# Kernel optimization log

Hardware: AMD Instinct MI355X
Metric: run time of the kernel (lower is better)

The kernel has to match this reference:

```python
import jax, jax.numpy as jnp
import numpy as np
import math

NUM_BINS, NUM_FREQS, NUM_KERNELS, MLP_HIDDEN = 128, 64, 3, 64
NUM_KEYS = 8192
ANCHORS = jnp.array([1000.0, 10000.0, 100000.0], dtype=jnp.float32)
LOG_ANCHORS = jnp.log10(ANCHORS)


def setup_inputs() -> dict:
    key = jax.random.key(0)
    ks = jax.random.split(key, 12)
    K = jax.random.normal(ks[0], (NUM_KEYS, 2 * NUM_FREQS), dtype=jnp.float32)
    key_positions = jax.random.randint(ks[1], (NUM_KEYS,), 0, 131072, dtype=jnp.int32)
    reference_angles = jax.random.normal(ks[2], (NUM_FREQS,), dtype=jnp.float32)
    # KernelEncodingLayer params
    centers = jnp.array([2 * math.pi * m / NUM_KERNELS - math.pi for m in range(NUM_KERNELS)], dtype=jnp.float32)
    mu = jax.random.normal(ks[3], (NUM_BINS, NUM_FREQS, NUM_KERNELS), dtype=jnp.float32) * 0.1 + centers
    kappa = jnp.ones((NUM_BINS, NUM_FREQS, NUM_KERNELS), dtype=jnp.float32)
    weight = jax.random.normal(ks[4], (NUM_BINS, NUM_FREQS, NUM_KERNELS), dtype=jnp.float32) * 0.1
    bias = jnp.zeros((NUM_BINS,), dtype=jnp.float32)
    # MLP params (kaiming-uniform-ish init)
    lim1 = 1.0 / math.sqrt(NUM_BINS)
    W1 = jax.random.uniform(ks[5], (MLP_HIDDEN, NUM_BINS), jnp.float32, -lim1, lim1)
    b1 = jax.random.uniform(ks[6], (MLP_HIDDEN,), jnp.float32, -lim1, lim1)
    lim2 = 1.0 / math.sqrt(MLP_HIDDEN)
    W2 = jax.random.uniform(ks[7], (1, MLP_HIDDEN), jnp.float32, -lim2, lim2)
    b2 = jax.random.uniform(ks[8], (1,), jnp.float32, -lim2, lim2)
    # PositionScalingLayer: softplus^-1(1.0)
    anchor_raw = jnp.full((3,), math.log(math.exp(1.0) - 1), dtype=jnp.float32)
    return {"K": K, "key_positions": key_positions, "reference_angles": reference_angles,
            "mu": mu, "kappa": kappa, "weight": weight, "bias": bias,
            "W1": W1, "b1": b1, "W2": W2, "b2": b2, "anchor_raw": anchor_raw}


def _position_weights(positions, anchor_raw):
    aw = jax.nn.softplus(anchor_raw)  # (3,)
    log_pos = jnp.log10(jnp.maximum(positions.astype(jnp.float32), 1.0))  # (N,)
    w = jnp.full_like(log_pos, aw[0])
    for i in range(LOG_ANCHORS.shape[0] - 1):
        ll, lr = LOG_ANCHORS[i], LOG_ANCHORS[i + 1]
        t = (log_pos - ll) / (lr - ll)
        interp = aw[i] * (1 - t) + aw[i + 1] * t
        w = jnp.where((log_pos >= ll) & (log_pos < lr), interp, w)
    w = jnp.where(log_pos >= LOG_ANCHORS[-1], aw[-1], w)
    return w


def reference(K, key_positions, reference_angles, mu, kappa, weight, bias, W1, b1, W2, b2, anchor_raw):
    N = K.shape[0]
    Kc = K.reshape(N, NUM_FREQS, 2)            # (N, F, 2)
    magnitude = jnp.linalg.norm(Kc, axis=2)     # (N, F)
    angle = jnp.arctan2(Kc[..., 1], Kc[..., 0])  # (N, F)
    mu_eff = mu + reference_angles[None, :, None]  # (B, F, M)
    # von Mises kernel: (N, B, F, M)
    kern = jnp.exp(kappa[None] * (jnp.cos(angle[:, None, :, None] - mu_eff[None]) - 1.0))
    wk = jnp.einsum('nbfm,bfm->nbf', kern, weight)       # sum over kernels
    logits = jnp.einsum('nbf,nf->nb', wk, magnitude) + bias  # (N, B)
    h = jax.nn.relu(logits @ W1.T + b1)
    mlp_out = (h @ W2.T + b2)[:, 0]            # (N,)
    pos_w = _position_weights(key_positions, anchor_raw)
    return jax.nn.sigmoid(mlp_out * pos_w)
```

## Files before the change

### kernel.cpp

```cpp
#include <hip/hip_runtime.h>
#include <math.h>

#define NBINS 128
#define NFREQ 64
#define NH    4
#define NSEG  (2*NH+1)
#define KDIM  (NSEG*NFREQ)
#define KSTEPS (KDIM/32)
#define ROWF  (KDIM+8)
#define ROWL  (NBINS+8)
#define ROWP  68

typedef _Float16 f16x8 __attribute__((ext_vector_type(8)));
typedef _Float16 f16x2 __attribute__((ext_vector_type(2)));
typedef float    f32x4 __attribute__((ext_vector_type(4)));

#define MFMA16(A,B,C) __builtin_amdgcn_mfma_f32_16x16x32_f16((A),(B),(C),0,0,0)

__global__ __launch_bounds__(256) void prep_kernel(
    const float* __restrict__ mu, const float* __restrict__ kappa,
    const float* __restrict__ weight, const float* __restrict__ ref,
    const float* __restrict__ W1,
    _Float16* __restrict__ Cfrag, _Float16* __restrict__ W1h)
{
    int u = blockIdx.x * 256 + threadIdx.x;
    W1h[u] = (_Float16)W1[u];

    int f = u >> 7;
    int bin = u & 127;
    float ra = ref[f];
    float A[NH + 1], B[NH + 1];
    #pragma unroll
    for (int k = 0; k <= NH; ++k) { A[k] = 0.f; B[k] = 0.f; }

    for (int m = 0; m < 3; ++m) {
        int idx = (bin * NFREQ + f) * 3 + m;
        float kap = kappa[idx];
        float wgt = weight[idx];
        float mue = mu[idx] + ra;
        float I[NH + 1];
        float x2 = kap * 0.5f, x2sq = x2 * x2;
        float fact = 1.f, xk = 1.f;
        #pragma unroll
        for (int k = 0; k <= NH; ++k) {
            if (k > 0) { fact *= (float)k; xk *= x2; }
            float term = xk / fact;
            float s = term;
            for (int j = 1; j <= 12; ++j) {
                term *= x2sq / ((float)j * (float)(j + k));
                s += term;
            }
            I[k] = s;
        }
        float e = expf(-kap) * wgt;
        float c1, s1; sincosf(mue, &s1, &c1);
        float ck = 1.f, sk = 0.f;
        A[0] += e * I[0];
        #pragma unroll
        for (int k = 1; k <= NH; ++k) {
            float cn = ck * c1 - sk * s1;
            float sn = sk * c1 + ck * s1;
            ck = cn; sk = sn;
            A[k] += e * 2.f * I[k] * ck;
            B[k] += e * 2.f * I[k] * sk;
        }
    }
    int bt = bin >> 4;
    #pragma unroll
    for (int seg = 0; seg < NSEG; ++seg) {
        float v = (seg == 0) ? A[0] : ((seg & 1) ? A[(seg + 1) >> 1] : B[seg >> 1]);
        int q = seg * NFREQ + f;
        int ks = q >> 5, kk = q & 31;
        int lane = (bin & 15) | (((kk >> 3) & 3) << 4);
        int elem = kk & 7;
        size_t flat = ((size_t)(ks * 8 + bt) * 64 + lane) * 8 + elem;
        Cfrag[flat] = (_Float16)v;
    }
}

__global__ __launch_bounds__(256) void main_kernel(
    const float* __restrict__ K, const int* __restrict__ kpos,
    const float* __restrict__ bias, const float* __restrict__ b1,
    const float* __restrict__ W2, const float* __restrict__ b2,
    const float* __restrict__ anchor_raw,
    const _Float16* __restrict__ Cfrag, const _Float16* __restrict__ W1h,
    float* __restrict__ out)
{
    __shared__ _Float16 PhiF[32 * ROWF];
    __shared__ _Float16 LgF[32 * ROWL];
    __shared__ float    Ps[32 * ROWP];
    __shared__ float    Pr[256];

    const int t  = threadIdx.x;
    const int n0 = blockIdx.x * 32;

    {
        int f2 = t & 31, krow = t >> 5;
        #pragma unroll
        for (int it = 0; it < 4; ++it) {
            int key = krow + 8 * it;
            float4 xy = *(const float4*)(K + (size_t)(n0 + key) * 128 + f2 * 4);
            float vs[2][NSEG];
            #pragma unroll
            for (int e = 0; e < 2; ++e) {
                float x = e ? xy.z : xy.x;
                float y = e ? xy.w : xy.y;
                float r2 = x * x + y * y;
                float inv = r2 > 0.f ? rsqrtf(r2) : 0.f;
                vs[e][0] = r2 * inv;
                float ca = x * inv, sa = y * inv;
                float mc = x, ms = y;
                vs[e][1] = mc; vs[e][2] = ms;
                #pragma unroll
                for (int h = 2; h <= NH; ++h) {
                    float mc2 = mc * ca - ms * sa;
                    float ms2 = ms * ca + mc * sa;
                    mc = mc2; ms = ms2;
                    vs[e][2 * h - 1] = mc; vs[e][2 * h] = ms;
                }
            }
            _Float16* dst = PhiF + key * ROWF + 2 * f2;
            #pragma unroll
            for (int s = 0; s < NSEG; ++s) {
                f16x2 pk; pk.x = (_Float16)vs[0][s]; pk.y = (_Float16)vs[1][s];
                *(f16x2*)(dst + s * 64) = pk;
            }
        }
    }
    __syncthreads();

    const int l = t & 63, w = t >> 6;
    f32x4 acc[2][2] = {};
    const _Float16* phA0 = PhiF + (l & 15) * ROWF + (l >> 4) * 8;
    const _Float16* phA1 = phA0 + 16 * ROWF;
    const _Float16* cb   = Cfrag + (size_t)(2 * w) * 512 + (size_t)l * 8;
    #define LA(PH, KS) (*(const f16x8*)((PH) + (KS) * 32))
    #define LB(KS, BT) (*(const f16x8*)(cb + ((size_t)(KS) * 8 + (BT)) * 512))

    f16x8 b00 = LB(0, 0), b01 = LB(0, 1), b10 = LB(1, 0), b11 = LB(1, 1);
    f16x8 a0 = LA(phA0, 0), a1 = LA(phA1, 0);
    #pragma unroll
    for (int ks = 0; ks < KSTEPS; ++ks) {
        int kb = ks + 2 < KSTEPS ? ks + 2 : ks;
        f16x8 nb0 = LB(kb, 0), nb1 = LB(kb, 1);
        int ka = ks + 1 < KSTEPS ? ks + 1 : ks;
        f16x8 na0 = LA(phA0, ka), na1 = LA(phA1, ka);
        acc[0][0] = MFMA16(a0, b00, acc[0][0]);
        acc[0][1] = MFMA16(a0, b01, acc[0][1]);
        acc[1][0] = MFMA16(a1, b00, acc[1][0]);
        acc[1][1] = MFMA16(a1, b01, acc[1][1]);
        a0 = na0; a1 = na1;
        b00 = b10; b01 = b11; b10 = nb0; b11 = nb1;
    }
    #undef LA
    #undef LB

    #pragma unroll
    for (int kt = 0; kt < 2; ++kt) {
        #pragma unroll
        for (int bt = 0; bt < 2; ++bt) {
            int bin = 32 * w + bt * 16 + (l & 15);
            float bb = bias[bin];
            #pragma unroll
            for (int r = 0; r < 4; ++r) {
                int key = kt * 16 + (l >> 4) * 4 + r;
                LgF[key * ROWL + bin] = (_Float16)(acc[kt][bt][r] + bb);
            }
        }
    }
    __syncthreads();

    f32x4 hacc[2] = {};
    const _Float16* lgA0 = LgF + (l & 15) * ROWL + (l >> 4) * 8;
    const _Float16* lgA1 = lgA0 + 16 * ROWL;
    const _Float16* wb   = W1h + (size_t)(16 * w + (l & 15)) * 128 + (l >> 4) * 8;
    #pragma unroll
    for (int ks = 0; ks < 4; ++ks) {
        f16x8 bfr = *(const f16x8*)(wb + ks * 32);
        f16x8 a0m = *(const f16x8*)(lgA0 + ks * 32);
        f16x8 a1m = *(const f16x8*)(lgA1 + ks * 32);
        hacc[0] = MFMA16(a0m, bfr, hacc[0]);
        hacc[1] = MFMA16(a1m, bfr, hacc[1]);
    }
    {
        int j = 16 * w + (l & 15);
        float b1j = b1[j], w2j = W2[j];
        #pragma unroll
        for (int kt = 0; kt < 2; ++kt) {
            #pragma unroll
            for (int r = 0; r < 4; ++r) {
                int key = kt * 16 + (l >> 4) * 4 + r;
                float h = hacc[kt][r] + b1j;
                Ps[key * ROWP + j] = fmaxf(h, 0.f) * w2j;
            }
        }
    }
    __syncthreads();

    {
        int key = t >> 3, g = t & 7;
        const float* p = Ps + key * ROWP + g * 8;
        Pr[t] = ((p[0] + p[1]) + (p[2] + p[3])) + ((p[4] + p[5]) + (p[6] + p[7]));
    }
    __syncthreads();
    if (t < 32) {
        const float* p = Pr + t * 8;
        float s = ((p[0] + p[1]) + (p[2] + p[3])) + ((p[4] + p[5]) + (p[6] + p[7]));
        float mlp = s + b2[0];
        float aw0 = log1pf(expf(anchor_raw[0]));
        float aw1 = log1pf(expf(anchor_raw[1]));
        float aw2 = log1pf(expf(anchor_raw[2]));
        int n = n0 + t;
        float pf = (float)kpos[n];
        float lp = log10f(fmaxf(pf, 1.f));
        float wgt;
        if      (lp < 3.f) wgt = aw0;
        else if (lp < 4.f) wgt = fmaf(aw1 - aw0, lp - 3.f, aw0);
        else if (lp < 5.f) wgt = fmaf(aw2 - aw1, lp - 4.f, aw1);
        else               wgt = aw2;
        float z = mlp * wgt;
        out[n] = 1.f / (1.f + expf(-z));
    }
}

extern "C" void kernel_launch(void* const* d_in, const int* in_sizes, int n_in,
                              void* d_out, int out_size, void* d_ws, size_t ws_size,
                              hipStream_t stream)
{
    const float* K    = (const float*)d_in[0];
    const int*   kpos = (const int*)d_in[1];
    const float* ref  = (const float*)d_in[2];
    const float* mu   = (const float*)d_in[3];
    const float* kap  = (const float*)d_in[4];
    const float* wgt  = (const float*)d_in[5];
    const float* bias = (const float*)d_in[6];
    const float* W1   = (const float*)d_in[7];
    const float* b1   = (const float*)d_in[8];
    const float* W2   = (const float*)d_in[9];
    const float* b2   = (const float*)d_in[10];
    const float* anc  = (const float*)d_in[11];
    float* out = (float*)d_out;

    int N = in_sizes[0] / (2 * NFREQ);

    char* ws = (char*)d_ws;
    _Float16* Cfrag = (_Float16*)ws;
    _Float16* W1h   = (_Float16*)(ws + 147456);

    prep_kernel<<<32, 256, 0, stream>>>(mu, kap, wgt, ref, W1, Cfrag, W1h);
    main_kernel<<<N / 32, 256, 0, stream>>>(K, kpos, bias, b1, W2, b2, anc,
                                            Cfrag, W1h, out);
}
```

Measured before the change: 91.11 us.

## Spread prep work across more blocks and halve keys per main block

The prep kernel now gives each von Mises kernel index its own thread (192 threads over 128 blocks) and sums the three contributions through shared memory. It also unrolls the Bessel series and replaces divisions with reciprocal constants. The main kernel handles 16 keys per block instead of 32, which doubles the grid to 512 blocks to fill the GPU's compute units better. In exchange, each block now reads the Cfrag B-fragments for half as many keys, so global reads of Cfrag are reused less.

Result: faster. 85.75 us (-5.9%).

```diff
diff --git a/kernel.cpp b/kernel.cpp
--- a/kernel.cpp
+++ b/kernel.cpp
@@ -17,64 +17,72 @@
 
 #define MFMA16(A,B,C) __builtin_amdgcn_mfma_f32_16x16x32_f16((A),(B),(C),0,0,0)
 
-__global__ __launch_bounds__(256) void prep_kernel(
+__global__ __launch_bounds__(192) void prep_kernel(
     const float* __restrict__ mu, const float* __restrict__ kappa,
     const float* __restrict__ weight, const float* __restrict__ ref,
     const float* __restrict__ W1,
     _Float16* __restrict__ Cfrag, _Float16* __restrict__ W1h)
 {
-    int u = blockIdx.x * 256 + threadIdx.x;
-    W1h[u] = (_Float16)W1[u];
-
-    int f = u >> 7;
-    int bin = u & 127;
-    float ra = ref[f];
-    float A[NH + 1], B[NH + 1];
-    #pragma unroll
-    for (int k = 0; k <= NH; ++k) { A[k] = 0.f; B[k] = 0.f; }
-
-    for (int m = 0; m < 3; ++m) {
-        int idx = (bin * NFREQ + f) * 3 + m;
-        float kap = kappa[idx];
-        float wgt = weight[idx];
-        float mue = mu[idx] + ra;
-        float I[NH + 1];
+    __shared__ float red[3][64][10];
+
+    const int t = threadIdx.x;
+    const int m = t >> 6;
+    const int g = t & 63;
+    const int G = blockIdx.x * 64 + g;
+    const int f = G & 63;
+
+    int wid = blockIdx.x * 192 + t;
+    if (wid < NBINS * 64) W1h[wid] = (_Float16)W1[wid];
+
+    const int idx = G * 3 + m;
+    float kap = kappa[idx];
+    float wgt = weight[idx];
+    float mue = mu[idx] + ref[f];
+
+    float I[NH + 1];
+    {
+        const float rfact[NH + 1] = {1.f, 1.f, 0.5f, 1.f / 6.f, 1.f / 24.f};
         float x2 = kap * 0.5f, x2sq = x2 * x2;
-        float fact = 1.f, xk = 1.f;
+        float xk = 1.f;
         #pragma unroll
         for (int k = 0; k <= NH; ++k) {
-            if (k > 0) { fact *= (float)k; xk *= x2; }
-            float term = xk / fact;
+            if (k > 0) xk *= x2;
+            float term = xk * rfact[k];
             float s = term;
+            #pragma unroll
             for (int j = 1; j <= 12; ++j) {
-                term *= x2sq / ((float)j * (float)(j + k));
+                term *= x2sq * (1.f / ((float)j * (float)(j + k)));
                 s += term;
             }
             I[k] = s;
         }
-        float e = expf(-kap) * wgt;
-        float c1, s1; sincosf(mue, &s1, &c1);
-        float ck = 1.f, sk = 0.f;
-        A[0] += e * I[0];
-        #pragma unroll
-        for (int k = 1; k <= NH; ++k) {
-            float cn = ck * c1 - sk * s1;
-            float sn = sk * c1 + ck * s1;
-            ck = cn; sk = sn;
-            A[k] += e * 2.f * I[k] * ck;
-            B[k] += e * 2.f * I[k] * sk;
-        }
-    }
-    int bt = bin >> 4;
-    #pragma unroll
-    for (int seg = 0; seg < NSEG; ++seg) {
-        float v = (seg == 0) ? A[0] : ((seg & 1) ? A[(seg + 1) >> 1] : B[seg >> 1]);
-        int q = seg * NFREQ + f;
-        int ks = q >> 5, kk = q & 31;
-        int lane = (bin & 15) | (((kk >> 3) & 3) << 4);
-        int elem = kk & 7;
-        size_t flat = ((size_t)(ks * 8 + bt) * 64 + lane) * 8 + elem;
-        Cfrag[flat] = (_Float16)v;
+    }
+    float e = expf(-kap) * wgt;
+    float c1, s1; sincosf(mue, &s1, &c1);
+    float ck = 1.f, sk = 0.f;
+    red[m][g][0] = e * I[0];
+    #pragma unroll
+    for (int k = 1; k <= NH; ++k) {
+        float cn = ck * c1 - sk * s1;
+        float sn = sk * c1 + ck * s1;
+        ck = cn; sk = sn;
+        red[m][g][2 * k - 1] = e * 2.f * I[k] * ck;
+        red[m][g][2 * k]     = e * 2.f * I[k] * sk;
+    }
+    __syncthreads();
+
+    if (t < 64) {
+        int G2 = blockIdx.x * 64 + t;
+        int bin = G2 >> 6, ff = G2 & 63, bt = bin >> 4;
+        #pragma unroll
+        for (int seg = 0; seg < NSEG; ++seg) {
+            float v = red[0][t][seg] + red[1][t][seg] + red[2][t][seg];
+            int q = seg * NFREQ + ff;
+            int ks = q >> 5, kk = q & 31;
+            int lane = (bin & 15) | (((kk >> 3) & 3) << 4);
+            int elem = kk & 7;
+            Cfrag[((size_t)(ks * 8 + bt) * 64 + lane) * 8 + elem] = (_Float16)v;
+        }
     }
 }
 
@@ -86,126 +94,113 @@
     const _Float16* __restrict__ Cfrag, const _Float16* __restrict__ W1h,
     float* __restrict__ out)
 {
-    __shared__ _Float16 PhiF[32 * ROWF];
-    __shared__ _Float16 LgF[32 * ROWL];
-    __shared__ float    Ps[32 * ROWP];
+    __shared__ _Float16 PhiF[16 * ROWF];
+    __shared__ _Float16 LgF[16 * ROWL];
+    __shared__ float    Ps[16 * ROWP];
     __shared__ float    Pr[256];
 
     const int t  = threadIdx.x;
-    const int n0 = blockIdx.x * 32;
-
-    {
-        int f2 = t & 31, krow = t >> 5;
-        #pragma unroll
-        for (int it = 0; it < 4; ++it) {
-            int key = krow + 8 * it;
-            float4 xy = *(const float4*)(K + (size_t)(n0 + key) * 128 + f2 * 4);
-            float vs[2][NSEG];
+    const int n0 = blockIdx.x * 16;
+
+    #pragma unroll
+    for (int it = 0; it < 2; ++it) {
+        int p = it * 256 + t;
+        int key = p >> 5, f2 = p & 31;
+        float4 xy = *(const float4*)(K + (size_t)(n0 + key) * 128 + f2 * 4);
+        float vs[2][NSEG];
+        #pragma unroll
+        for (int e = 0; e < 2; ++e) {
+            float x = e ? xy.z : xy.x;
+            float y = e ? xy.w : xy.y;
+            float r2 = x * x + y * y;
+            float inv = r2 > 0.f ? rsqrtf(r2) : 0.f;
+            vs[e][0] = r2 * inv;
+            float ca = x * inv, sa = y * inv;
+            float mc = x, ms = y;
+            vs[e][1] = mc; vs[e][2] = ms;
             #pragma unroll
-            for (int e = 0; e < 2; ++e) {
-                float x = e ? xy.z : xy.x;
-                float y = e ? xy.w : xy.y;
-                float r2 = x * x + y * y;
-                float inv = r2 > 0.f ? rsqrtf(r2) : 0.f;
-                vs[e][0] = r2 * inv;
-                float ca = x * inv, sa = y * inv;
-                float mc = x, ms = y;
-                vs[e][1] = mc; vs[e][2] = ms;
-                #pragma unroll
-                for (int h = 2; h <= NH; ++h) {
-                    float mc2 = mc * ca - ms * sa;
-                    float ms2 = ms * ca + mc * sa;
-                    mc = mc2; ms = ms2;
-                    vs[e][2 * h - 1] = mc; vs[e][2 * h] = ms;
-                }
+            for (int h = 2; h <= NH; ++h) {
+                float mc2 = mc * ca - ms * sa;
+                float ms2 = ms * ca + mc * sa;
+                mc = mc2; ms = ms2;
+                vs[e][2 * h - 1] = mc; vs[e][2 * h] = ms;
             }
-            _Float16* dst = PhiF + key * ROWF + 2 * f2;
-            #pragma unroll
-            for (int s = 0; s < NSEG; ++s) {
-                f16x2 pk; pk.x = (_Float16)vs[0][s]; pk.y = (_Float16)vs[1][s];
-                *(f16x2*)(dst + s * 64) = pk;
-            }
+        }
+        _Float16* dst = PhiF + key * ROWF + 2 * f2;
+        #pragma unroll
+        for (int s = 0; s < NSEG; ++s) {
+            f16x2 pk; pk.x = (_Float16)vs[0][s]; pk.y = (_Float16)vs[1][s];
+            *(f16x2*)(dst + s * 64) = pk;
         }
     }
     __syncthreads();
 
     const int l = t & 63, w = t >> 6;
-    f32x4 acc[2][2] = {};
-    const _Float16* phA0 = PhiF + (l & 15) * ROWF + (l >> 4) * 8;
-    const _Float16* phA1 = phA0 + 16 * ROWF;
-    const _Float16* cb   = Cfrag + (size_t)(2 * w) * 512 + (size_t)l * 8;
-    #define LA(PH, KS) (*(const f16x8*)((PH) + (KS) * 32))
+    f32x4 acc[2] = {};
+    const _Float16* phA = PhiF + (l & 15) * ROWF + (l >> 4) * 8;
+    const _Float16* cb  = Cfrag + (size_t)(2 * w) * 512 + (size_t)l * 8;
+    #define LA(KS) (*(const f16x8*)(phA + (KS) * 32))
     #define LB(KS, BT) (*(const f16x8*)(cb + ((size_t)(KS) * 8 + (BT)) * 512))
 
     f16x8 b00 = LB(0, 0), b01 = LB(0, 1), b10 = LB(1, 0), b11 = LB(1, 1);
-    f16x8 a0 = LA(phA0, 0), a1 = LA(phA1, 0);
+    f16x8 a0 = LA(0);
     #pragma unroll
     for (int ks = 0; ks < KSTEPS; ++ks) {
-        int kb = ks + 2 < KSTEPS ? ks + 2 : ks;
+        int kb = ks + 2 < KSTEPS ? ks + 2 : KSTEPS - 1;
         f16x8 nb0 = LB(kb, 0), nb1 = LB(kb, 1);
-        int ka = ks + 1 < KSTEPS ? ks + 1 : ks;
-        f16x8 na0 = LA(phA0, ka), na1 = LA(phA1, ka);
-        acc[0][0] = MFMA16(a0, b00, acc[0][0]);
-        acc[0][1] = MFMA16(a0, b01, acc[0][1]);
-        acc[1][0] = MFMA16(a1, b00, acc[1][0]);
-        acc[1][1] = MFMA16(a1, b01, acc[1][1]);
-        a0 = na0; a1 = na1;
+        int ka = ks + 1 < KSTEPS ? ks + 1 : KSTEPS - 1;
+        f16x8 na0 = LA(ka);
+        acc[0] = MFMA16(a0, b00, acc[0]);
+        acc[1] = MFMA16(a0, b01, acc[1]);
+        a0 = na0;
         b00 = b10; b01 = b11; b10 = nb0; b11 = nb1;
     }
     #undef LA
     #undef LB
 
     #pragma unroll
-    for (int kt = 0; kt < 2; ++kt) {
-        #pragma unroll
-        for (int bt = 0; bt < 2; ++bt) {
-            int bin = 32 * w + bt * 16 + (l & 15);
-            float bb = bias[bin];
-            #pragma unroll
-            for (int r = 0; r < 4; ++r) {
-                int key = kt * 16 + (l >> 4) * 4 + r;
-                LgF[key * ROWL + bin] = (_Float16)(acc[kt][bt][r] + bb);
-            }
-        }
-    }
-    __syncthreads();
-
-    f32x4 hacc[2] = {};
-    const _Float16* lgA0 = LgF + (l & 15) * ROWL + (l >> 4) * 8;
-    const _Float16* lgA1 = lgA0 + 16 * ROWL;
-    const _Float16* wb   = W1h + (size_t)(16 * w + (l & 15)) * 128 + (l >> 4) * 8;
+    for (int bt = 0; bt < 2; ++bt) {
+        int bin = 32 * w + bt * 16 + (l & 15);
+        float bbv = bias[bin];
+        #pragma unroll
+        for (int r = 0; r < 4; ++r) {
+            int key = (l >> 4) * 4 + r;
+            LgF[key * ROWL + bin] = (_Float16)(acc[bt][r] + bbv);
+        }
+    }
+    __syncthreads();
+
+    f32x4 hacc = {};
+    const _Float16* lgA = LgF + (l & 15) * ROWL + (l >> 4) * 8;
+    const _Float16* wb  = W1h + (size_t)(16 * w + (l & 15)) * 128 + (l >> 4) * 8;
     #pragma unroll
     for (int ks = 0; ks < 4; ++ks) {
         f16x8 bfr = *(const f16x8*)(wb + ks * 32);
-        f16x8 a0m = *(const f16x8*)(lgA0 + ks * 32);
-        f16x8 a1m = *(const f16x8*)(lgA1 + ks * 32);
-        hacc[0] = MFMA16(a0m, bfr, hacc[0]);
-        hacc[1] = MFMA16(a1m, bfr, hacc[1]);
+        f16x8 am  = *(const f16x8*)(lgA + ks * 32);
+        hacc = MFMA16(am, bfr, hacc);
     }
     {
         int j = 16 * w + (l & 15);
         float b1j = b1[j], w2j = W2[j];
         #pragma unroll
-        for (int kt = 0; kt < 2; ++kt) {
-            #pragma unroll
-            for (int r = 0; r < 4; ++r) {
-                int key = kt * 16 + (l >> 4) * 4 + r;
-                float h = hacc[kt][r] + b1j;
-                Ps[key * ROWP + j] = fmaxf(h, 0.f) * w2j;
-            }
+        for (int r = 0; r < 4; ++r) {
+            int key = (l >> 4) * 4 + r;
+            float h = hacc[r] + b1j;
+            Ps[key * ROWP + j] = fmaxf(h, 0.f) * w2j;
         }
     }
     __syncthreads();
 
     {
-        int key = t >> 3, g = t & 7;
-        const float* p = Ps + key * ROWP + g * 8;
-        Pr[t] = ((p[0] + p[1]) + (p[2] + p[3])) + ((p[4] + p[5]) + (p[6] + p[7]));
-    }
-    __syncthreads();
-    if (t < 32) {
-        const float* p = Pr + t * 8;
-        float s = ((p[0] + p[1]) + (p[2] + p[3])) + ((p[4] + p[5]) + (p[6] + p[7]));
+        int key = t >> 4, gg = t & 15;
+        const float* p = Ps + key * ROWP + gg * 4;
+        Pr[t] = (p[0] + p[1]) + (p[2] + p[3]);
+    }
+    __syncthreads();
+    if (t < 16) {
+        const float* p = Pr + t * 16;
+        float s = (((p[0] + p[1]) + (p[2] + p[3])) + ((p[4] + p[5]) + (p[6] + p[7])))
+                + (((p[8] + p[9]) + (p[10] + p[11])) + ((p[12] + p[13]) + (p[14] + p[15])));
         float mlp = s + b2[0];
         float aw0 = log1pf(expf(anchor_raw[0]));
         float aw1 = log1pf(expf(anchor_raw[1]));
@@ -247,7 +242,7 @@
     _Float16* Cfrag = (_Float16*)ws;
     _Float16* W1h   = (_Float16*)(ws + 147456);
 
-    prep_kernel<<<32, 256, 0, stream>>>(mu, kap, wgt, ref, W1, Cfrag, W1h);
-    main_kernel<<<N / 32, 256, 0, stream>>>(K, kpos, bias, b1, W2, b2, anc,
+    prep_kernel<<<128, 192, 0, stream>>>(mu, kap, wgt, ref, W1, Cfrag, W1h);
+    main_kernel<<<N / 16, 256, 0, stream>>>(K, kpos, bias, b1, W2, b2, anc,
                                             Cfrag, W1h, out);
 }
```
